# Performance work log

Hardware: AMD Instinct MI355X
Metric: run time of the kernel (lower is better)

Reference implementation:

```python
import jax, jax.numpy as jnp
import numpy as np

B, T, D = 4, 4096, 1024
N_DOCS, TOP_K, HEADS = 4096, 8, 4
EPS = 1e-12  # matches F.normalize default eps


def setup_inputs() -> dict:
    key = jax.random.key(0)
    ks = jax.random.split(key, 14)
    f = jnp.float32
    s = D ** -0.5
    return {
        "x": jax.random.normal(ks[0], (B, T, D), f),
        "hex_weights": jax.random.normal(ks[1], (B, T, 64), f),
        "doc_keys": jax.random.normal(ks[2], (N_DOCS, 64), f) * 0.1,
        "doc_values": jax.random.normal(ks[3], (N_DOCS, D), f) * 0.1,
        "Wq_hex": jax.random.normal(ks[4], (64, 64), f) * 0.125,
        "Wq": jax.random.normal(ks[5], (D, D), f) * s,
        "Wk": jax.random.normal(ks[6], (D, D), f) * s,
        "Wv": jax.random.normal(ks[7], (D, D), f) * s,
        "bq": jnp.zeros((D,), f),
        "bk": jnp.zeros((D,), f),
        "bv": jnp.zeros((D,), f),
        "Wo": jax.random.normal(ks[8], (D, D), f) * s,
        "bo": jnp.zeros((D,), f),
        "W_doc": jax.random.normal(ks[9], (D, D), f) * s,
        "gate": jnp.zeros((1,), f),
    }


def _l2norm(v):
    return v / jnp.maximum(jnp.linalg.norm(v, axis=-1, keepdims=True), EPS)


def reference(x, hex_weights, doc_keys, doc_values, Wq_hex, Wq, Wk, Wv,
              bq, bk, bv, Wo, bo, W_doc, gate):
    # --- retrieve: cosine similarity in 64-dim hexagram space ---
    q = hex_weights @ Wq_hex                      # (B,T,64)
    sim = jnp.einsum('bth,nh->btn', _l2norm(q), _l2norm(doc_keys))  # (B,T,N_DOCS)
    top_scores, top_idx = jax.lax.top_k(sim, TOP_K)  # (B,T,K)

    # --- gather + softmax-weighted combine ---
    doc_vals = doc_values[top_idx]                # (B,T,K,D) irregular gather
    attn_w = jax.nn.softmax(top_scores, axis=-1)  # (B,T,K)
    retrieved = jnp.einsum('btk,btkd->btd', attn_w, doc_vals)  # (B,T,D)
    doc_context = retrieved @ W_doc               # (B,T,D)

    # --- degenerate cross-attention: q len 1, kv len 1 per token ---
    # softmax over a single key is exactly 1, so attention output = v;
    # q/k projections contribute nothing (and have zero gradient), matching torch.
    v = doc_context @ Wv + bv                     # (B,T,D)
    out = v @ Wo + bo                             # out_proj

    return x + jax.nn.sigmoid(gate) * out
```

## Files before the change

kernel.cpp:

```cpp
#include <hip/hip_runtime.h>
#include <math.h>

#define NTOK  16384
#define DDIM  1024
#define NDOCS 4096
#define NSLICE 8
#define SLICE (NDOCS/NSLICE)
#define TOPL  6
#define CPT   (NSLICE*4*TOPL)
#define MN20  (1u<<20)

typedef __attribute__((ext_vector_type(8))) short short8;
typedef __attribute__((ext_vector_type(4))) float f32x4;

__device__ __forceinline__ float b2f(unsigned short u){
  union { unsigned int i; float f; } v; v.i = ((unsigned int)u) << 16; return v.f;
}
__device__ __forceinline__ unsigned short f2b(float f){
  union { float f; unsigned int i; } v; v.f = f;
  unsigned int r = v.i + 0x7fffu + ((v.i >> 16) & 1u);
  return (unsigned short)(r >> 16);
}
__device__ __forceinline__ void gld16(const void* g, void* l){
  __builtin_amdgcn_global_load_lds(
      (const __attribute__((address_space(1))) void*)g,
      (__attribute__((address_space(3))) void*)l, 16, 0, 0);
}
__device__ __forceinline__ void kinsert(unsigned int* keys, unsigned int key){
  #pragma unroll
  for (int k = TOPL-1; k >= 1; --k){
    unsigned int lo = keys[k-1] < key ? keys[k-1] : key;
    keys[k] = keys[k] > lo ? keys[k] : lo;
  }
  keys[0] = keys[0] > key ? keys[0] : key;
}

__global__ __launch_bounds__(256)
void prep_kernel(const float* __restrict__ dvals, unsigned short* __restrict__ dv16,
                 const float* __restrict__ Wdoc,  unsigned short* __restrict__ wd16,
                 const float* __restrict__ Wv,    unsigned short* __restrict__ T1,
                 const float* __restrict__ Wo,    unsigned short* __restrict__ T2,
                 const float* __restrict__ bv, const float* __restrict__ bo,
                 float* __restrict__ bc){
  __shared__ unsigned short t[32][33];
  __shared__ float part[4][64];
  int bx = blockIdx.x, tid = threadIdx.x;
  if (bx < 5120){
    const float* in        = bx < 4096 ? dvals : Wdoc;
    unsigned short* outp   = bx < 4096 ? dv16  : wd16;
    size_t base = (size_t)(bx < 4096 ? bx : bx - 4096) * 1024;
    size_t i = base + (size_t)tid * 4;
    float4 v = *(const float4*)(in + i);
    ushort4 o; o.x = f2b(v.x); o.y = f2b(v.y); o.z = f2b(v.z); o.w = f2b(v.w);
    *(ushort4*)(outp + i) = o;
  } else if (bx < 7168){
    int b = bx - 5120;
    const float* in      = b < 1024 ? Wv : Wo;
    unsigned short* outp = b < 1024 ? T1 : T2;
    b &= 1023;
    int c0 = (b & 31) * 32, r0 = (b >> 5) * 32;
    int lc = tid & 31, lr = tid >> 5;
    #pragma unroll
    for (int i = 0; i < 4; i++){
      int r = lr + i*8;
      t[r][lc] = f2b(in[(size_t)(r0 + r)*DDIM + c0 + lc]);
    }
    __syncthreads();
    #pragma unroll
    for (int i = 0; i < 4; i++){
      int r = lr + i*8;
      outp[(size_t)(c0 + r)*DDIM + r0 + lc] = t[lc][r];
    }
  } else {
    int b = bx - 7168;
    int lane = tid & 63, w = tid >> 6;
    int n = b * 64 + lane;
    float acc = 0.f;
    int k0 = w * 256;
    for (int k = k0; k < k0 + 256; k++)
      acc += bv[k] * Wo[(size_t)k*DDIM + n];
    part[w][lane] = acc;
    __syncthreads();
    if (w == 0)
      bc[n] = part[0][lane] + part[1][lane] + part[2][lane] + part[3][lane] + bo[n];
  }
}

__global__ __launch_bounds__(256)
void norm_kernel(const float* __restrict__ hexw, const float* __restrict__ Wq,
                 float* __restrict__ qn, const float* __restrict__ dkeys,
                 float* __restrict__ dkn, unsigned short* __restrict__ dkn16s){
  __shared__ float Wsh[64*64];
  __shared__ float hx[4][64];
  int bx = blockIdx.x, tid = threadIdx.x;
  int w = tid >> 6, j = tid & 63;
  if (bx < 4096){
    #pragma unroll
    for (int i = 0; i < 16; i++){ int e = tid + i*256; Wsh[e] = Wq[e]; }
    int t = bx * 4 + w;
    hx[w][j] = hexw[(size_t)t*64 + j];
    __syncthreads();
    float s = 0.f;
    #pragma unroll
    for (int h = 0; h < 64; h++) s += hx[w][h] * Wsh[h*64 + j];
    float ss = s*s;
    #pragma unroll
    for (int off = 32; off >= 1; off >>= 1) ss += __shfl_xor(ss, off, 64);
    qn[(size_t)t*64 + j] = s / fmaxf(sqrtf(ss), 1e-12f);
  } else {
    int t = (bx - 4096) * 4 + w;
    float v = dkeys[(size_t)t*64 + j];
    float ss = v*v;
    #pragma unroll
    for (int off = 32; off >= 1; off >>= 1) ss += __shfl_xor(ss, off, 64);
    float o = v / fmaxf(sqrtf(ss), 1e-12f);
    dkn[(size_t)t*64 + j] = o;
    dkn16s[((size_t)(t >> 5) << 11) + ((j >> 3) << 8) + ((t & 31) << 3) + (j & 7)] = f2b(o);
  }
}

__global__ __launch_bounds__(256)
void topk_part(const float* __restrict__ qn, const unsigned short* __restrict__ dkn16s,
               unsigned int* __restrict__ kbuf){
  __shared__ __align__(16) unsigned short buf[2][2048];
  int tid  = threadIdx.x;
  int wv   = tid >> 6;
  int lane = tid & 63;
  int tl   = lane & 15;
  int g    = lane >> 4;
  int token = blockIdx.x*64 + wv*16 + tl;
  int dbase = blockIdx.y * SLICE;
  int T0    = dbase >> 5;

  const float* qrow = qn + (size_t)token*64 + g*8;
  float4 u0 = *(const float4*)(qrow);
  float4 u1 = *(const float4*)(qrow + 4);
  float4 v0 = *(const float4*)(qrow + 32);
  float4 v1 = *(const float4*)(qrow + 36);
  short8 q0 = (short8){(short)f2b(u0.x),(short)f2b(u0.y),(short)f2b(u0.z),(short)f2b(u0.w),
                       (short)f2b(u1.x),(short)f2b(u1.y),(short)f2b(u1.z),(short)f2b(u1.w)};
  short8 q1 = (short8){(short)f2b(v0.x),(short)f2b(v0.y),(short)f2b(v0.z),(short)f2b(v0.w),
                       (short)f2b(v1.x),(short)f2b(v1.y),(short)f2b(v1.z),(short)f2b(v1.w)};

  unsigned int keysA[TOPL], keysB[TOPL];
  #pragma unroll
  for (int k = 0; k < TOPL; k++){ keysA[k] = 0u; keysB[k] = 0u; }
  const unsigned int HI = 0xFFFF0000u;
  unsigned int idlow0 = 4095u - (unsigned)(dbase + g*4);

  gld16(dkn16s + ((size_t)T0 << 11) + wv*512 + lane*8, &buf[0][wv*512]);
  __syncthreads();

  #pragma unroll 2
  for (int it = 0; it < SLICE/32; ++it){
    int cur = it & 1;
    if (it < SLICE/32 - 1)
      gld16(dkn16s + ((size_t)(T0 + it + 1) << 11) + wv*512 + lane*8,
            &buf[cur ^ 1][wv*512]);

    const unsigned short* bp = &buf[cur][0];
    short8 a0 = *(const short8*)(bp + g*256        + tl*8);
    short8 a1 = *(const short8*)(bp + (g+4)*256    + tl*8);
    short8 b0 = *(const short8*)(bp + g*256 + 128  + tl*8);
    short8 b1 = *(const short8*)(bp + (g+4)*256 + 128 + tl*8);

    f32x4 accA = (f32x4){3.0f, 3.0f, 3.0f, 3.0f};
    f32x4 accB = (f32x4){3.0f, 3.0f, 3.0f, 3.0f};
    accA = __builtin_amdgcn_mfma_f32_16x16x32_bf16(a0, q0, accA, 0, 0, 0);
    accB = __builtin_amdgcn_mfma_f32_16x16x32_bf16(b0, q0, accB, 0, 0, 0);
    accA = __builtin_amdgcn_mfma_f32_16x16x32_bf16(a1, q1, accA, 0, 0, 0);
    accB = __builtin_amdgcn_mfma_f32_16x16x32_bf16(b1, q1, accB, 0, 0, 0);

    unsigned int ibA = idlow0 - (unsigned)(it*32);
    unsigned int ibB = ibA - 16u;
    #pragma unroll
    for (int r = 0; r < 4; ++r){
      unsigned int kA = (((__float_as_uint(accA[r]) << 8) - 0xC0000000u) & HI)
                      | (ibA - (unsigned)r);
      unsigned int kB = (((__float_as_uint(accB[r]) << 8) - 0xC0000000u) & HI)
                      | (ibB - (unsigned)r);
      kinsert(keysA, kA);
      kinsert(keysB, kB);
    }
    __syncthreads();
  }

  #pragma unroll
  for (int k = 0; k < TOPL; ++k) kinsert(keysA, keysB[k]);

  size_t base = (size_t)token*CPT + (size_t)blockIdx.y*(4*TOPL) + (size_t)g*TOPL;
  #pragma unroll
  for (int k = 0; k < TOPL; k += 2)
    *(uint2*)&kbuf[base + k] = (uint2){keysA[k], keysA[k+1]};
}

__global__ __launch_bounds__(256)
void topk_rescore(const unsigned int* __restrict__ kbuf, const float* __restrict__ qn,
                  const float* __restrict__ dkn, float* __restrict__ wsm,
                  int* __restrict__ idx){
  __shared__ unsigned int smid[4][16];
  __shared__ float       ssc[4][16];
  int tid = threadIdx.x, wv = tid >> 6, lane = tid & 63;
  int t = blockIdx.x * 4 + wv;

  const unsigned int* kp = kbuf + (size_t)t*CPT;
  unsigned int k0 = kp[lane], k1 = kp[lane+64], k2 = kp[lane+128];
  unsigned int a;
  if (k1 > k0){ a = k0; k0 = k1; k1 = a; }
  if (k2 > k1){ a = k1; k1 = k2; k2 = a; }
  if (k1 > k0){ a = k0; k0 = k1; k1 = a; }

  int h = 0;
  #pragma unroll
  for (int r = 0; r < 16; ++r){
    unsigned int cand = (h == 0) ? k0 : ((h == 1) ? k1 : ((h == 2) ? k2 : 0u));
    unsigned int m = cand;
    #pragma unroll
    for (int off = 1; off < 64; off <<= 1){
      unsigned int o = __shfl_xor(m, off, 64);
      m = (m > o) ? m : o;
    }
    if (cand == m && h < 3) h++;
    if (lane == 0) smid[wv][r] = m;
  }
  __syncthreads();

  int cnum = lane >> 2, sub = lane & 3;
  unsigned int mk = smid[wv][cnum];
  int did = 4095 - (int)(mk & 0xFFFFu);
  const float4* kr = (const float4*)(dkn + (size_t)did*64 + sub*16);
  const float4* qp = (const float4*)(qn  + (size_t)t*64   + sub*16);
  float s = 0.f;
  #pragma unroll
  for (int c = 0; c < 4; ++c){
    float4 kv = kr[c], qv = qp[c];
    s += qv.x*kv.x + qv.y*kv.y + qv.z*kv.z + qv.w*kv.w;
  }
  s += __shfl_xor(s, 1, 64);
  s += __shfl_xor(s, 2, 64);
  if (sub == 0) ssc[wv][cnum] = s;
  __syncthreads();

  if (lane == 0){
    float sc[16]; int ids[16];
    #pragma unroll
    for (int i = 0; i < 16; ++i){
      sc[i]  = ssc[wv][i];
      ids[i] = 4095 - (int)(smid[wv][i] & 0xFFFFu);
    }
    float ws[8]; int wid[8];
    #pragma unroll
    for (int r = 0; r < 8; ++r){
      float bs = sc[0]; int bi = ids[0];
      #pragma unroll
      for (int i = 1; i < 16; ++i)
        if (sc[i] > bs || (sc[i] == bs && ids[i] < bi)){ bs = sc[i]; bi = ids[i]; }
      ws[r] = bs; wid[r] = bi;
      #pragma unroll
      for (int i = 0; i < 16; ++i) if (ids[i] == bi) sc[i] = -1e30f;
    }
    float e[8], sum = 0.f;
    #pragma unroll
    for (int k = 0; k < 8; ++k){ e[k] = expf(ws[k] - ws[0]); sum += e[k]; }
    float inv = 1.f / sum;
    #pragma unroll
    for (int k = 0; k < 8; ++k){
      wsm[(size_t)t*8 + k] = e[k] * inv;
      idx[(size_t)t*8 + k] = wid[k];
    }
  }
}

template<int TSTORE, int PARTIAL>
__global__ __launch_bounds__(256)
void gemm_bt_kernel(const unsigned short* __restrict__ A, const unsigned short* __restrict__ Bt,
                    void* __restrict__ C, int M, int N, int K){
  __shared__ __align__(16) short As[128*32];
  __shared__ __align__(16) short Bs[128*32];
  int tid  = threadIdx.x;
  int lane = tid & 63;
  int wv   = tid >> 6;
  int wm = wv & 1, wn = wv >> 1;
  size_t bm = (size_t)blockIdx.x * 128, bn = (size_t)blockIdx.y * 128;
  int klen = K / (int)gridDim.z;
  int kz0  = (int)blockIdx.z * klen;

  f32x4 acc[4][4];
  #pragma unroll
  for (int i = 0; i < 4; i++)
    #pragma unroll
    for (int j = 0; j < 4; j++) acc[i][j] = (f32x4){0.f, 0.f, 0.f, 0.f};

  size_t aoff = (bm + (size_t)(tid >> 2))*K + (tid & 3)*8 + kz0;
  size_t boff = (bn + (size_t)(tid >> 2))*K + (tid & 3)*8 + kz0;

  for (int k0 = 0; k0 < klen; k0 += 32){
    __syncthreads();
    gld16(A  + aoff + k0,                 &As[wv*512]);
    gld16(A  + aoff + (size_t)64*K + k0,  &As[2048 + wv*512]);
    gld16(Bt + boff + k0,                 &Bs[wv*512]);
    gld16(Bt + boff + (size_t)64*K + k0,  &Bs[2048 + wv*512]);
    __syncthreads();

    short8 af[4], bf[4];
    int kb = (lane >> 4) * 8;
    int rA = wm*64 + (lane & 15);
    int rB = wn*64 + (lane & 15);
    #pragma unroll
    for (int i = 0; i < 4; i++) af[i] = *(const short8*)&As[(rA + i*16)*32 + kb];
    #pragma unroll
    for (int i = 0; i < 4; i++) bf[i] = *(const short8*)&Bs[(rB + i*16)*32 + kb];
    #pragma unroll
    for (int i = 0; i < 4; i++)
      #pragma unroll
      for (int j = 0; j < 4; j++)
        acc[i][j] = __builtin_amdgcn_mfma_f32_16x16x32_bf16(af[i], bf[j], acc[i][j], 0, 0, 0);
  }

  int ci = lane & 15, rg = lane >> 4;
  #pragma unroll
  for (int i = 0; i < 4; i++)
    #pragma unroll
    for (int j = 0; j < 4; j++)
      #pragma unroll
      for (int r = 0; r < 4; r++){
        size_t row = bm + wm*64 + i*16 + rg*4 + r;
        size_t col = bn + wn*64 + j*16 + ci;
        size_t e = TSTORE ? (col*(size_t)M + row) : (row*(size_t)N + col);
        if (PARTIAL) ((float*)C)[(size_t)blockIdx.z*M*N + e] = acc[i][j][r];
        else         ((unsigned short*)C)[e] = f2b(acc[i][j][r]);
      }
}

__global__ __launch_bounds__(256)
void reduce4_bf16(const float* __restrict__ p, unsigned short* __restrict__ o){
  size_t i = ((size_t)blockIdx.x * 256 + threadIdx.x) * 4;
  float4 a0 = *(const float4*)(p + i);
  float4 a1 = *(const float4*)(p + i + (size_t)MN20);
  float4 a2 = *(const float4*)(p + i + (size_t)2*MN20);
  float4 a3 = *(const float4*)(p + i + (size_t)3*MN20);
  ushort4 r;
  r.x = f2b(a0.x + a1.x + a2.x + a3.x);
  r.y = f2b(a0.y + a1.y + a2.y + a3.y);
  r.z = f2b(a0.z + a1.z + a2.z + a3.z);
  r.w = f2b(a0.w + a1.w + a2.w + a3.w);
  *(ushort4*)(o + i) = r;
}

__global__ __launch_bounds__(256)
void output_kernel(const float* __restrict__ x, const float* __restrict__ wsm,
                   const int* __restrict__ idx, const unsigned short* __restrict__ P,
                   const float* __restrict__ bc, const float* __restrict__ gate,
                   float* __restrict__ out){
  __shared__ float ws8[8]; __shared__ int is8[8];
  int t = blockIdx.x, tid = threadIdx.x;
  if (tid < 8){
    ws8[tid] = wsm[(size_t)t*8 + tid];
    int ii = idx[(size_t)t*8 + tid];
    is8[tid] = ii < 0 ? 0 : (ii > NDOCS-1 ? NDOCS-1 : ii);
  }
  __syncthreads();
  float g = 1.f / (1.f + expf(-gate[0]));
  int c = tid * 4;
  float a0 = 0.f, a1 = 0.f, a2 = 0.f, a3 = 0.f;
  #pragma unroll
  for (int k = 0; k < 8; k++){
    ushort4 u = *(const ushort4*)(P + (size_t)is8[k]*DDIM + c);
    float w = ws8[k];
    a0 += w * b2f(u.x); a1 += w * b2f(u.y); a2 += w * b2f(u.z); a3 += w * b2f(u.w);
  }
  float4 xf = *(const float4*)(x + (size_t)t*DDIM + c);
  float4 o;
  o.x = xf.x + g * (a0 + bc[c]);
  o.y = xf.y + g * (a1 + bc[c+1]);
  o.z = xf.z + g * (a2 + bc[c+2]);
  o.w = xf.w + g * (a3 + bc[c+3]);
  *(float4*)(out + (size_t)t*DDIM + c) = o;
}

__global__ __launch_bounds__(256)
void zero_out_kernel(float* __restrict__ out){
  size_t i = ((size_t)blockIdx.x * 256 + threadIdx.x) * 4;
  *(float4*)(out + i) = (float4){0.f,0.f,0.f,0.f};
}

extern "C" void kernel_launch(void* const* d_in, const int* in_sizes, int n_in,
                              void* d_out, int out_size, void* d_ws, size_t ws_size,
                              hipStream_t stream){
  (void)in_sizes; (void)n_in; (void)out_size;
  const float* x     = (const float*)d_in[0];
  const float* hexw  = (const float*)d_in[1];
  const float* dkeys = (const float*)d_in[2];
  const float* dvals = (const float*)d_in[3];
  const float* Wqh   = (const float*)d_in[4];
  const float* Wv    = (const float*)d_in[7];
  const float* bv    = (const float*)d_in[10];
  const float* Wo    = (const float*)d_in[11];
  const float* bo    = (const float*)d_in[12];
  const float* Wdoc  = (const float*)d_in[13];
  const float* gate  = (const float*)d_in[14];
  float* out = (float*)d_out;

  const size_t NEED = ((size_t)22 << 20) + 4096;
  if (ws_size < NEED){
    zero_out_kernel<<<NTOK*DDIM/1024, 256, 0, stream>>>(out);
    return;
  }

  char* ws = (char*)d_ws;
  float* qn             = (float*)(ws);
  float* dkn            = (float*)(ws + ((size_t)4 << 20));
  float* wsm            = (float*)(ws + ((size_t)5 << 20));
  int*   idx            = (int*)  (ws + ((size_t)5 << 20) + (512 << 10));
  unsigned short* T1    = (unsigned short*)(ws + ((size_t)6  << 20));
  unsigned short* T2    = (unsigned short*)(ws + ((size_t)8  << 20));
  unsigned short* tmp   = (unsigned short*)(ws + ((size_t)10 << 20));
  unsigned short* WcT   = (unsigned short*)(ws + ((size_t)12 << 20));
  unsigned short* P     = (unsigned short*)(ws + ((size_t)14 << 20));
  unsigned short* dkn16s= (unsigned short*)(ws + ((size_t)12 << 20));
  float* bc             = (float*)(ws + ((size_t)22 << 20));
  char* dob             = (char*)d_out;
  float*          pbuf = (float*)dob;
  unsigned int*   kbuf = (unsigned int*)dob;
  unsigned short* dv16 = (unsigned short*)(dob + ((size_t)16 << 20));
  unsigned short* wd16 = (unsigned short*)(dob + ((size_t)24 << 20));

  prep_kernel<<<7184, 256, 0, stream>>>(dvals, dv16, Wdoc, wd16, Wv, T1, Wo, T2,
                                        bv, bo, bc);
  gemm_bt_kernel<0,1><<<dim3(8,8,4),  256, 0, stream>>>(wd16, T1, pbuf, DDIM, DDIM, DDIM);
  reduce4_bf16<<<1024, 256, 0, stream>>>(pbuf, tmp);
  gemm_bt_kernel<1,1><<<dim3(8,8,4),  256, 0, stream>>>(tmp,  T2, pbuf, DDIM, DDIM, DDIM);
  reduce4_bf16<<<1024, 256, 0, stream>>>(pbuf, WcT);
  gemm_bt_kernel<0,0><<<dim3(32,8,1), 256, 0, stream>>>(dv16, WcT, P, NDOCS, DDIM, DDIM);

  norm_kernel<<<4096 + NDOCS/4, 256, 0, stream>>>(hexw, Wqh, qn, dkeys, dkn, dkn16s);
  topk_part<<<dim3(NTOK/64, NSLICE), 256, 0, stream>>>(qn, dkn16s, kbuf);
  topk_rescore<<<NTOK/4, 256, 0, stream>>>(kbuf, qn, dkn, wsm, idx);

  output_kernel<<<NTOK, 256, 0, stream>>>(x, wsm, idx, P, bc, gate, out);
}
```

Measured before the change: 356.6 us.

## Merge per-group top-k candidates in-wavefront and rank-sort in rescore kernel

The similarity kernel now merges the four per-group top-6 candidate lists in registers using shuffles and bitonic-8 networks, writing only 8 keys per slice instead of 24. This shrinks the candidate buffer from 192 to 64 keys per token. The rescore kernel replaces the iterative 16-round wave-max extraction with a single rank-by-counting pass over 64 keys. The final serial top-8 selection on lane 0 becomes a parallel rank computation across 16 lanes. The risk is that the merge keeps only the top 8 per slice where up to 24 were kept before, which could change candidate recall near ties.

```diff
diff --git a/kernel.cpp b/kernel.cpp
--- a/kernel.cpp
+++ b/kernel.cpp
@@ -7,7 +7,7 @@
 #define NSLICE 8
 #define SLICE (NDOCS/NSLICE)
 #define TOPL  6
-#define CPT   (NSLICE*4*TOPL)
+#define KPT   64
 #define MN20  (1u<<20)
 
 typedef __attribute__((ext_vector_type(8))) short short8;
@@ -33,6 +33,14 @@
     keys[k] = keys[k] > lo ? keys[k] : lo;
   }
   keys[0] = keys[0] > key ? keys[0] : key;
+}
+__device__ __forceinline__ void ceswap(unsigned int& a, unsigned int& b){
+  unsigned int mx = a > b ? a : b, mn = a > b ? b : a; a = mx; b = mn;
+}
+__device__ __forceinline__ void bitonic8(unsigned int* c){
+  ceswap(c[0],c[4]); ceswap(c[1],c[5]); ceswap(c[2],c[6]); ceswap(c[3],c[7]);
+  ceswap(c[0],c[2]); ceswap(c[1],c[3]); ceswap(c[4],c[6]); ceswap(c[5],c[7]);
+  ceswap(c[0],c[1]); ceswap(c[2],c[3]); ceswap(c[4],c[5]); ceswap(c[6],c[7]);
 }
 
 __global__ __launch_bounds__(256)
@@ -188,10 +196,30 @@
   #pragma unroll
   for (int k = 0; k < TOPL; ++k) kinsert(keysA, keysB[k]);
 
-  size_t base = (size_t)token*CPT + (size_t)blockIdx.y*(4*TOPL) + (size_t)g*TOPL;
-  #pragma unroll
-  for (int k = 0; k < TOPL; k += 2)
-    *(uint2*)&kbuf[base + k] = (uint2){keysA[k], keysA[k+1]};
+  unsigned int pb[TOPL], c[8];
+  #pragma unroll
+  for (int j = 0; j < TOPL; ++j) pb[j] = __shfl_xor(keysA[j], 16, 64);
+  c[0] = keysA[0];
+  c[1] = keysA[1];
+  c[2] = keysA[2] > pb[5] ? keysA[2] : pb[5];
+  c[3] = keysA[3] > pb[4] ? keysA[3] : pb[4];
+  c[4] = keysA[4] > pb[3] ? keysA[4] : pb[3];
+  c[5] = keysA[5] > pb[2] ? keysA[5] : pb[2];
+  c[6] = pb[1];
+  c[7] = pb[0];
+  bitonic8(c);
+  unsigned int pc[8], d[8];
+  #pragma unroll
+  for (int j = 0; j < 8; ++j) pc[j] = __shfl_xor(c[j], 32, 64);
+  #pragma unroll
+  for (int j = 0; j < 8; ++j) d[j] = c[j] > pc[7-j] ? c[j] : pc[7-j];
+  bitonic8(d);
+
+  if (g == 0){
+    size_t base = (size_t)token*KPT + (size_t)blockIdx.y*8;
+    *(uint4*)&kbuf[base]     = (uint4){d[0], d[1], d[2], d[3]};
+    *(uint4*)&kbuf[base + 4] = (uint4){d[4], d[5], d[6], d[7]};
+  }
 }
 
 __global__ __launch_bounds__(256)
@@ -203,26 +231,14 @@
   int tid = threadIdx.x, wv = tid >> 6, lane = tid & 63;
   int t = blockIdx.x * 4 + wv;
 
-  const unsigned int* kp = kbuf + (size_t)t*CPT;
-  unsigned int k0 = kp[lane], k1 = kp[lane+64], k2 = kp[lane+128];
-  unsigned int a;
-  if (k1 > k0){ a = k0; k0 = k1; k1 = a; }
-  if (k2 > k1){ a = k1; k1 = k2; k2 = a; }
-  if (k1 > k0){ a = k0; k0 = k1; k1 = a; }
-
-  int h = 0;
-  #pragma unroll
-  for (int r = 0; r < 16; ++r){
-    unsigned int cand = (h == 0) ? k0 : ((h == 1) ? k1 : ((h == 2) ? k2 : 0u));
-    unsigned int m = cand;
-    #pragma unroll
-    for (int off = 1; off < 64; off <<= 1){
-      unsigned int o = __shfl_xor(m, off, 64);
-      m = (m > o) ? m : o;
-    }
-    if (cand == m && h < 3) h++;
-    if (lane == 0) smid[wv][r] = m;
-  }
+  unsigned int k = kbuf[(size_t)t*KPT + lane];
+  int rank = 0;
+  #pragma unroll
+  for (int i = 0; i < 64; ++i){
+    unsigned int o = __shfl(k, i, 64);
+    rank += (o > k) ? 1 : 0;
+  }
+  if (rank < 16) smid[wv][rank] = k;
   __syncthreads();
 
   int cnum = lane >> 2, sub = lane & 3;
@@ -241,33 +257,26 @@
   if (sub == 0) ssc[wv][cnum] = s;
   __syncthreads();
 
-  if (lane == 0){
-    float sc[16]; int ids[16];
-    #pragma unroll
-    for (int i = 0; i < 16; ++i){
-      sc[i]  = ssc[wv][i];
-      ids[i] = 4095 - (int)(smid[wv][i] & 0xFFFFu);
-    }
-    float ws[8]; int wid[8];
-    #pragma unroll
-    for (int r = 0; r < 8; ++r){
-      float bs = sc[0]; int bi = ids[0];
-      #pragma unroll
-      for (int i = 1; i < 16; ++i)
-        if (sc[i] > bs || (sc[i] == bs && ids[i] < bi)){ bs = sc[i]; bi = ids[i]; }
-      ws[r] = bs; wid[r] = bi;
-      #pragma unroll
-      for (int i = 0; i < 16; ++i) if (ids[i] == bi) sc[i] = -1e30f;
-    }
-    float e[8], sum = 0.f;
-    #pragma unroll
-    for (int k = 0; k < 8; ++k){ e[k] = expf(ws[k] - ws[0]); sum += e[k]; }
+  float sc = (lane < 16) ? ssc[wv][lane] : -1e30f;
+  int   id = (lane < 16) ? (4095 - (int)(smid[wv][lane] & 0xFFFFu)) : 0x7fffffff;
+  int r2 = 0;
+  #pragma unroll
+  for (int i = 0; i < 16; ++i){
+    float os = __shfl(sc, i, 64);
+    int   oi = __shfl(id, i, 64);
+    r2 += (os > sc || (os == sc && oi < id)) ? 1 : 0;
+  }
+  float mx = sc;
+  #pragma unroll
+  for (int off = 1; off < 64; off <<= 1) mx = fmaxf(mx, __shfl_xor(mx, off, 64));
+  float e = (lane < 16 && r2 < 8) ? expf(sc - mx) : 0.f;
+  float sum = e;
+  #pragma unroll
+  for (int off = 1; off < 64; off <<= 1) sum += __shfl_xor(sum, off, 64);
+  if (lane < 16 && r2 < 8){
     float inv = 1.f / sum;
-    #pragma unroll
-    for (int k = 0; k < 8; ++k){
-      wsm[(size_t)t*8 + k] = e[k] * inv;
-      idx[(size_t)t*8 + k] = wid[k];
-    }
+    wsm[(size_t)t*8 + r2] = e * inv;
+    idx[(size_t)t*8 + r2] = id;
   }
 }
 
```

After: 328.1 us. -8.0%, faster.
